# Kernel tuning notes

Hardware: AMD Instinct MI355X
Metric: run time of the kernel (lower is better)

Reference implementation:

```python
import jax, jax.numpy as jnp
import numpy as np

B, C, H, W = 16, 256, 96, 96
CQ = C // 8      # 32, query/key channels in CrossAttention
CM = C // 2      # 128, inter_planes


def conv1x1(x, w, b=None):
    # x: [B,Cin,H,W], w: [Cout,Cin]
    y = jnp.einsum('bchw,oc->bohw', x, w)
    if b is not None:
        y = y + b[None, :, None, None]
    return y


def cross_attention(x, wq, bq, wk, bk, wv, bv, gamma):
    # criss-cross (axial H and W) attention with -inf diagonal on the H branch
    b_, c_, h_, w_ = x.shape
    q = conv1x1(x, wq, bq)  # [B,CQ,H,W]
    k = conv1x1(x, wk, bk)
    v = conv1x1(x, wv, bv)  # [B,C,H,W]
    # energy over column (H axis): [B,H,W,H], masked diag h==h'
    e_h = jnp.einsum('bchw,bckw->bhwk', q, k)
    diag = jnp.eye(h_, dtype=bool)[None, :, None, :]  # [1,H,1,H]
    e_h = jnp.where(diag, -jnp.inf, e_h)
    # energy over row (W axis): [B,H,W,W]
    e_w = jnp.einsum('bchw,bchv->bhwv', q, k)
    att = jax.nn.softmax(jnp.concatenate([e_h, e_w], axis=3), axis=3)
    a_h, a_w = att[..., :h_], att[..., h_:]
    out_h = jnp.einsum('bckw,bhwk->bchw', v, a_h)
    out_w = jnp.einsum('bchv,bhwv->bchw', v, a_w)
    return gamma * (out_h + out_w) + x


def spatial_weighted(x, w_q_right, w_v_right, w_up, b_up):
    b_, _, h_, w_ = x.shape
    inp = conv1x1(x, w_v_right).reshape(b_, CM, h_ * w_)        # [B,CM,HW]
    mask = conv1x1(x, w_q_right).reshape(b_, 1, h_ * w_)        # [B,1,HW]
    mask = jax.nn.softmax(mask, axis=2)
    ctx = jnp.einsum('bcn,bon->bco', inp, mask)                 # [B,CM,1]
    ctx = jnp.einsum('bci,oc->boi', ctx, w_up) + b_up[None, :, None]  # [B,C,1]
    mask_ch = jax.nn.sigmoid(ctx)[..., None]                    # [B,C,1,1]
    return x * mask_ch


def channel_weighted(x, w_q_left, w_v_left):
    b_, _, h_, w_ = x.shape
    g = conv1x1(x, w_q_left)                                    # [B,CM,H,W]
    avg = jnp.mean(g, axis=(2, 3))                              # [B,CM]
    theta = conv1x1(x, w_v_left).reshape(b_, CM, h_ * w_)       # [B,CM,HW]
    ctx = jnp.einsum('bc,bcn->bn', avg, theta)                  # [B,HW]
    ctx = jax.nn.softmax(ctx, axis=1).reshape(b_, 1, h_, w_)
    return x * jax.nn.sigmoid(ctx)


def setup_inputs() -> dict:
    key = jax.random.key(0)
    ks = jax.random.split(key, 16)
    s = lambda fan_in: (2.0 / fan_in) ** 0.5
    inp = {
        'x': jax.random.normal(ks[0], (B, C, H, W), jnp.float32),
        'w_q_right': jax.random.normal(ks[1], (1, C), jnp.float32) * s(C),
        'w_v_right': jax.random.normal(ks[2], (CM, C), jnp.float32) * s(C),
        'w_up': jax.random.normal(ks[3], (C, CM), jnp.float32) * s(CM),
        'b_up': jnp.zeros((C,), jnp.float32),
        'w_q_left': jax.random.normal(ks[4], (CM, C), jnp.float32) * s(C),
        'w_v_left': jax.random.normal(ks[5], (CM, C), jnp.float32) * s(C),
        'cr_wq': jax.random.normal(ks[6], (CQ, C), jnp.float32) * s(C),
        'cr_bq': jnp.zeros((CQ,), jnp.float32),
        'cr_wk': jax.random.normal(ks[7], (CQ, C), jnp.float32) * s(C),
        'cr_bk': jnp.zeros((CQ,), jnp.float32),
        'cr_wv': jax.random.normal(ks[8], (C, C), jnp.float32) * s(C),
        'cr_bv': jnp.zeros((C,), jnp.float32),
        'gamma': jax.random.normal(ks[9], (1,), jnp.float32) * 0.1,
    }
    return inp


def reference(x, w_q_right, w_v_right, w_up, b_up, w_q_left, w_v_left,
              cr_wq, cr_bq, cr_wk, cr_bk, cr_wv, cr_bv, gamma):
    cross = lambda t: cross_attention(t, cr_wq, cr_bq, cr_wk, cr_bk, cr_wv, cr_bv, gamma)
    ctx_channel = cross(spatial_weighted(x, w_q_right, w_v_right, w_up, b_up))
    ctx_spatial = cross(channel_weighted(x, w_q_left, w_v_left))
    return cross(ctx_spatial + ctx_channel)
```

## Files before the change

kernel.cpp:

```cpp
#include <hip/hip_runtime.h>
#include <math.h>

#define Bn 16
#define Cn 256
#define CQn 32
#define CMn 128
#define Hn 96
#define Wn 96
#define Nn 9216
#define PIXn 147456

typedef short bf8 __attribute__((ext_vector_type(8)));
typedef float f32x4 __attribute__((ext_vector_type(4)));
#define MFMA(a,b,c) __builtin_amdgcn_mfma_f32_16x16x32_bf16(a,b,c,0,0,0)

typedef unsigned short ushort_t;

__device__ inline ushort_t f2bf(float f){
  union{float f; unsigned int u;} v; v.f=f;
  unsigned int r = v.u + 0x7fffu + ((v.u>>16)&1u);
  return (ushort_t)(r>>16);
}
__device__ inline float bf2f(ushort_t s){
  union{unsigned int u; float f;} v; v.u = ((unsigned int)s)<<16;
  return v.f;
}

__device__ inline float waveSum(float v){
#pragma unroll
  for(int o=32;o;o>>=1) v += __shfl_down(v,o,64);
  return v;
}
__device__ inline float waveMax(float v){
#pragma unroll
  for(int o=32;o;o>>=1) v = fmaxf(v,__shfl_down(v,o,64));
  return v;
}


__global__ __launch_bounds__(1024) void k_pass1(const float* __restrict__ x,
    const float* __restrict__ wqr, float* __restrict__ xmean,
    float* __restrict__ partp){
  int cg = blockIdx.x, b = blockIdx.y, tid = threadIdx.x;
  __shared__ float r16[16];
  float mp[9];
#pragma unroll
  for(int k=0;k<9;k++) mp[k]=0.f;
  for(int cc=0;cc<16;cc++){
    int c = cg*16+cc;
    const float* row = x + ((size_t)b*Cn + c)*Nn;
    float w = wqr[c];
    float s = 0.f;
#pragma unroll
    for(int k=0;k<9;k++){
      float v = row[k*1024+tid];
      s += v;
      mp[k] += w*v;
    }
    s = waveSum(s);
    if((tid&63)==0) r16[tid>>6]=s;
    __syncthreads();
    if(tid==0){
      float t=0.f;
      for(int i=0;i<16;i++) t+=r16[i];
      xmean[(size_t)b*Cn + c] = t*(1.f/Nn);
    }
    __syncthreads();
  }
  float* dst = partp + ((size_t)cg*Bn + b)*Nn;
#pragma unroll
  for(int k=0;k<9;k++) dst[k*1024+tid]=mp[k];
}

__global__ __launch_bounds__(1024) void k_pass2(const float* __restrict__ x,
    const float* __restrict__ wvec, const float* __restrict__ maskb,
    float* __restrict__ xw, float* __restrict__ partp){
  int cg = blockIdx.x, b = blockIdx.y, tid = threadIdx.x;
  __shared__ float r16[16];
  float cp[9], mk[9];
#pragma unroll
  for(int k=0;k<9;k++){
    cp[k]=0.f;
    mk[k]=maskb[(size_t)b*Nn + k*1024+tid];
  }
  for(int cc=0;cc<16;cc++){
    int c = cg*16+cc;
    const float* row = x + ((size_t)b*Cn + c)*Nn;
    float w = wvec[(size_t)b*Cn + c];
    float s = 0.f;
#pragma unroll
    for(int k=0;k<9;k++){
      float v = row[k*1024+tid];
      s += mk[k]*v;
      cp[k] += w*v;
    }
    s = waveSum(s);
    if((tid&63)==0) r16[tid>>6]=s;
    __syncthreads();
    if(tid==0){
      float t=0.f;
      for(int i=0;i<16;i++) t+=r16[i];
      xw[(size_t)b*Cn + c] = t;
    }
    __syncthreads();
  }
  float* dst = partp + ((size_t)cg*Bn + b)*Nn;
#pragma unroll
  for(int k=0;k<9;k++) dst[k*1024+tid]=cp[k];
}

__global__ void k_red16(const float* __restrict__ part, float* __restrict__ out){
  size_t p = (size_t)blockIdx.x*256 + threadIdx.x;
  float s=0.f;
#pragma unroll
  for(int cg=0;cg<16;cg++) s += part[(size_t)cg*Bn*Nn + p];
  out[p]=s;
}

__global__ void k_small1(const float* __restrict__ xmean, const float* __restrict__ wql,
                         const float* __restrict__ wvl, float* __restrict__ wvec){
  int b=blockIdx.x, t=threadIdx.x;
  __shared__ float xm[Cn];
  __shared__ float av[CMn];
  xm[t] = xmean[b*Cn+t];
  __syncthreads();
  if(t<CMn){
    float s=0.f;
    for(int c=0;c<Cn;c++) s += wql[t*Cn+c]*xm[c];
    av[t]=s;
  }
  __syncthreads();
  float s=0.f;
  for(int m=0;m<CMn;m++) s += av[m]*wvl[m*Cn+t];
  wvec[b*Cn+t]=s;
}

__global__ void k_softmax_n(const float* __restrict__ in, float* __restrict__ out, int mode){
  int b=blockIdx.x, tid=threadIdx.x, lane=tid&63, wid=tid>>6;
  const float* p = in + (size_t)b*Nn;
  __shared__ float red[16];
  __shared__ float bc2[2];
  float mx=-3e38f;
  for(int i=tid;i<Nn;i+=1024) mx=fmaxf(mx,p[i]);
  mx = waveMax(mx);
  if(lane==0) red[wid]=mx;
  __syncthreads();
  if(tid==0){ float m=red[0]; for(int i=1;i<16;i++) m=fmaxf(m,red[i]); bc2[0]=m; }
  __syncthreads();
  mx=bc2[0];
  float s=0.f;
  for(int i=tid;i<Nn;i+=1024) s+=expf(p[i]-mx);
  s = waveSum(s);
  __syncthreads();
  if(lane==0) red[wid]=s;
  __syncthreads();
  if(tid==0){ float t=0.f; for(int i=0;i<16;i++) t+=red[i]; bc2[1]=t; }
  __syncthreads();
  float inv=1.f/bc2[1];
  for(int i=tid;i<Nn;i+=1024){
    float e=expf(p[i]-mx)*inv;
    out[(size_t)b*Nn+i] = mode ? 1.f/(1.f+expf(-e)) : e;
  }
}

__global__ void k_small2(const float* __restrict__ xw, const float* __restrict__ wvr,
                         const float* __restrict__ wup, const float* __restrict__ bup,
                         float* __restrict__ g1){
  int b=blockIdx.x, t=threadIdx.x;
  __shared__ float xs[Cn];
  __shared__ float cx[CMn];
  xs[t]=xw[b*Cn+t];
  __syncthreads();
  if(t<CMn){
    float s=0.f;
    for(int c=0;c<Cn;c++) s += wvr[t*Cn+c]*xs[c];
    cx[t]=s;
  }
  __syncthreads();
  float s=bup[t];
  for(int m=0;m<CMn;m++) s += wup[t*CMn+m]*cx[m];
  g1[b*Cn+t]=1.f/(1.f+expf(-s));
}

__global__ void k_gates(const float* __restrict__ x, const float* __restrict__ g1,
                        const float* __restrict__ m2, ushort_t* __restrict__ t1,
                        ushort_t* __restrict__ t2){
  size_t i4 = ((size_t)blockIdx.x*256 + threadIdx.x)*4;
  int n  = (int)(i4 % Nn);
  int bc = (int)(i4 / Nn);
  int b  = bc / Cn;
  float4 xv = *(const float4*)&x[i4];
  float g = g1[bc];
  float4 mv = *(const float4*)&m2[(size_t)b*Nn + n];
  uint2 a, c;
  a.x = (unsigned)f2bf(xv.x*g) | ((unsigned)f2bf(xv.y*g)<<16);
  a.y = (unsigned)f2bf(xv.z*g) | ((unsigned)f2bf(xv.w*g)<<16);
  c.x = (unsigned)f2bf(xv.x*mv.x) | ((unsigned)f2bf(xv.y*mv.y)<<16);
  c.y = (unsigned)f2bf(xv.z*mv.z) | ((unsigned)f2bf(xv.w*mv.w)<<16);
  *(uint2*)&t1[i4] = a;
  *(uint2*)&t2[i4] = c;
}

__global__ void k_add_bf(ushort_t* __restrict__ a, const ushort_t* __restrict__ b){
  size_t i = ((size_t)blockIdx.x*256 + threadIdx.x)*8;
  uint4 av = *(const uint4*)&a[i];
  uint4 bv = *(const uint4*)&b[i];
  unsigned* ap = (unsigned*)&av; unsigned* bp2 = (unsigned*)&bv;
  uint4 ov;
  unsigned* op = (unsigned*)&ov;
#pragma unroll
  for(int k=0;k<4;k++){
    float lo = bf2f((ushort_t)(ap[k]&0xffff)) + bf2f((ushort_t)(bp2[k]&0xffff));
    float hi = bf2f((ushort_t)(ap[k]>>16))    + bf2f((ushort_t)(bp2[k]>>16));
    op[k] = (unsigned)f2bf(lo) | ((unsigned)f2bf(hi)<<16);
  }
  *(uint4*)&a[i] = ov;
}


__global__ void k_packb(const float* __restrict__ wq, const float* __restrict__ bq,
                        const float* __restrict__ wk, const float* __restrict__ bk,
                        const float* __restrict__ wv, const float* __restrict__ bv,
                        ushort_t* __restrict__ Wp, float* __restrict__ bp){
  int o = blockIdx.x, t = threadIdx.x;
  const float* src; float bs;
  if(o<32){ src = wq + o*Cn; bs = bq[o]; }
  else if(o<64){ src = wk + (o-32)*Cn; bs = bk[o-32]; }
  else { src = wv + (o-64)*Cn; bs = bv[o-64]; }
  Wp[o*Cn+t] = f2bf(src[t]);
  if(t==0) bp[o] = bs;
}

#define AP 40
#define BP 264

__global__ __launch_bounds__(256) void k_gemm_qkv(const ushort_t* __restrict__ x,
    const ushort_t* __restrict__ Wp, const float* __restrict__ bp,
    ushort_t* __restrict__ Yqk, ushort_t* __restrict__ Vb){
  __shared__ ushort_t Ws[320*AP];
  __shared__ ushort_t Bt[64*BP];
  int b  = blockIdx.y;
  int n0 = blockIdx.x*64;
  int tid = threadIdx.x, lane = tid&63, wid = tid>>6;

  {
    const ushort_t* xb = x + (size_t)b*Cn*Nn + n0 + (tid&63);
    int cg = (tid>>6)*8;
#pragma unroll
    for(int p=0;p<8;p++){
      int c8 = p*32 + cg;
      unsigned e0=xb[(size_t)(c8+0)*Nn], e1=xb[(size_t)(c8+1)*Nn];
      unsigned e2=xb[(size_t)(c8+2)*Nn], e3=xb[(size_t)(c8+3)*Nn];
      unsigned e4=xb[(size_t)(c8+4)*Nn], e5=xb[(size_t)(c8+5)*Nn];
      unsigned e6=xb[(size_t)(c8+6)*Nn], e7=xb[(size_t)(c8+7)*Nn];
      uint4 pk;
      pk.x = e0 | (e1<<16); pk.y = e2 | (e3<<16);
      pk.z = e4 | (e5<<16); pk.w = e6 | (e7<<16);
      *(uint4*)&Bt[(tid&63)*BP + c8] = pk;
    }
  }

  f32x4 acc[5][4];
#pragma unroll
  for(int f=0;f<5;f++)
#pragma unroll
    for(int g=0;g<4;g++) acc[f][g] = (f32x4){0.f,0.f,0.f,0.f};

  for(int ki=0;ki<8;ki++){
    __syncthreads();
#pragma unroll
    for(int q=0;q<5;q++){
      int fidx = q*256 + tid;
      int o = fidx>>2, kk = (fidx&3)*8;
      uint4 wv = *(const uint4*)&Wp[o*Cn + ki*32 + kk];
      *(uint4*)&Ws[o*AP + kk] = wv;
    }
    __syncthreads();
    bf8 bfr[4];
#pragma unroll
    for(int g=0;g<4;g++)
      bfr[g] = *(const bf8*)&Bt[(g*16 + (lane&15))*BP + ki*32 + (lane>>4)*8];
#pragma unroll
    for(int f=0;f<5;f++){
      bf8 a = *(const bf8*)&Ws[(wid*80 + f*16 + (lane&15))*AP + (lane>>4)*8];
#pragma unroll
      for(int g=0;g<4;g++) acc[f][g] = MFMA(a, bfr[g], acc[f][g]);
    }
  }

#pragma unroll
  for(int f=0;f<5;f++){
    int ob = wid*80 + f*16 + (lane>>4)*4;
#pragma unroll
    for(int i=0;i<4;i++){
      int o = ob + i;
      float bias = bp[o];
      ushort_t* dst = (o<64) ? (Yqk + ((size_t)b*64 + o)*Nn)
                             : (Vb + ((size_t)b*Cn + (o-64))*Nn);
#pragma unroll
      for(int g=0;g<4;g++)
        dst[n0 + g*16 + (lane&15)] = f2bf(acc[f][g][i] + bias);
    }
  }
}

__global__ __launch_bounds__(256) void k_transpose_b(const ushort_t* __restrict__ src,
                                                     ushort_t* __restrict__ dst){
  __shared__ ushort_t Ls[96*98];
  size_t base = (size_t)blockIdx.x * Nn;
  int tid = threadIdx.x;
  for(int e=tid*2; e<Nn; e+=512){
    unsigned int u = *(const unsigned int*)&src[base+e];
    int r=e/96, c=e%96;
    *(unsigned int*)&Ls[r*98+c] = u;
  }
  __syncthreads();
  for(int e=tid*2; e<Nn; e+=512){
    int r=e/96, c=e%96;
    unsigned int u = (unsigned int)Ls[c*98+r] | (((unsigned int)Ls[(c+1)*98+r])<<16);
    *(unsigned int*)&dst[base+e] = u;
  }
}

__global__ __launch_bounds__(256) void k_e(const ushort_t* __restrict__ Y,
    float* __restrict__ att, int aoff, int diag, int pm, int pr){
  __shared__ ushort_t Qt[96*AP];
  __shared__ ushort_t Kt[96*AP];
  int bid = blockIdx.x; int b = bid/96, r = bid%96;
  int tid = threadIdx.x, lane = tid&63, wid = tid>>6;
  {
    int half = tid>>7;
    int cg   = (tid>>5)&3;
    int l32  = tid&31;
    ushort_t* T = half ? Kt : Qt;
    const ushort_t* S = Y + ((size_t)b*64 + half*32 + cg*8)*Nn + (size_t)r*96;
#pragma unroll
    for(int p=0;p<3;p++){
      int sp = p*32 + l32;
      unsigned e0=S[(size_t)0*Nn+sp], e1=S[(size_t)1*Nn+sp];
      unsigned e2=S[(size_t)2*Nn+sp], e3=S[(size_t)3*Nn+sp];
      unsigned e4=S[(size_t)4*Nn+sp], e5=S[(size_t)5*Nn+sp];
      unsigned e6=S[(size_t)6*Nn+sp], e7=S[(size_t)7*Nn+sp];
      uint4 pk;
      pk.x = e0 | (e1<<16); pk.y = e2 | (e3<<16);
      pk.z = e4 | (e5<<16); pk.w = e6 | (e7<<16);
      *(uint4*)&T[sp*AP + cg*8] = pk;
    }
  }
  __syncthreads();
  int mb = (wid>>1)*48, nb = (wid&1)*48;
  const f32x4 z4 = {0.f,0.f,0.f,0.f};
  f32x4 acc[3][3];
  bf8 a[3], bb[3];
#pragma unroll
  for(int f=0;f<3;f++) a[f] = *(const bf8*)&Qt[(mb+f*16+(lane&15))*AP + (lane>>4)*8];
#pragma unroll
  for(int g=0;g<3;g++) bb[g] = *(const bf8*)&Kt[(nb+g*16+(lane&15))*AP + (lane>>4)*8];
#pragma unroll
  for(int f=0;f<3;f++)
#pragma unroll
    for(int g=0;g<3;g++) acc[f][g] = MFMA(a[f], bb[g], z4);
#pragma unroll
  for(int f=0;f<3;f++)
#pragma unroll
    for(int i=0;i<4;i++){
      int m = mb + f*16 + (lane>>4)*4 + i;
      float* arow = att + ((size_t)b*Nn + (size_t)m*pm + (size_t)r*pr)*192 + aoff;
#pragma unroll
      for(int g=0;g<3;g++){
        int n = nb + g*16 + (lane&15);
        arow[n] = (diag && n==m) ? -1e30f : acc[f][g][i];
      }
    }
}

__global__ void k_softmax_att(const float* __restrict__ att, ushort_t* __restrict__ attb){
  int wave = threadIdx.x>>6, lane = threadIdx.x&63;
  size_t p = (size_t)blockIdx.x*4 + wave;
  const float* a = att + p*192;
  float v0=a[lane], v1=a[lane+64], v2=a[lane+128];
  float mx = fmaxf(v0, fmaxf(v1,v2));
#pragma unroll
  for(int o=32;o;o>>=1) mx = fmaxf(mx, __shfl_xor(mx,o,64));
  float e0=expf(v0-mx), e1=expf(v1-mx), e2=expf(v2-mx);
  float s=e0+e1+e2;
#pragma unroll
  for(int o=32;o;o>>=1) s += __shfl_xor(s,o,64);
  float inv=1.f/s;
  ushort_t* ob = attb + p*192;
  ob[lane]     = f2bf(e0*inv);
  ob[lane+64]  = f2bf(e1*inv);
  ob[lane+128] = f2bf(e2*inv);
}

#define SP 120

template<int MODE, int OUTF>
__global__ __launch_bounds__(256) void k_pv(const ushort_t* V,
    const ushort_t* __restrict__ attb, const ushort_t* resid,
    float* __restrict__ Of, ushort_t* Ob, const float* __restrict__ gp){
  __shared__ ushort_t As[96*SP];
  int r = blockIdx.x, ch2 = blockIdx.y, b = blockIdx.z;
  float gm = gp[0];
  int tid = threadIdx.x, lane = tid&63, wid = tid>>6;
  size_t vbase = (size_t)b*Cn*Nn + (size_t)r*96;
  bf8 vf[6];
#pragma unroll
  for(int f=0;f<2;f++)
#pragma unroll
    for(int j=0;j<3;j++)
      vf[f*3+j] = *(const bf8*)&V[vbase
        + (size_t)(ch2*128 + wid*32 + f*16 + (lane&15))*Nn + j*32 + (lane>>4)*8];
  const ushort_t* ab = attb + (size_t)b*Nn*192
                     + (MODE ? (size_t)r*192 : (size_t)r*96*192 + 96);
  const size_t arow = MODE ? (size_t)96*192 : (size_t)192;
  for(int u=tid; u<96*12; u+=256){
    int n=u/12, j8=(u%12)*8;
    uint4 q = *(const uint4*)&ab[(size_t)n*arow + j8];
    *(uint4*)&As[n*SP + j8] = q;
  }
  __syncthreads();
  f32x4 acc[2][6];
#pragma unroll
  for(int f=0;f<2;f++)
#pragma unroll
    for(int g=0;g<6;g++) acc[f][g] = (f32x4){0.f,0.f,0.f,0.f};
#pragma unroll
  for(int j0=0;j0<3;j0++){
    bf8 bfr[6];
#pragma unroll
    for(int g=0;g<6;g++)
      bfr[g] = *(const bf8*)&As[(g*16+(lane&15))*SP + j0*32 + (lane>>4)*8];
#pragma unroll
    for(int f=0;f<2;f++)
#pragma unroll
      for(int g=0;g<6;g++) acc[f][g] = MFMA(vf[f*3+j0], bfr[g], acc[f][g]);
  }
#pragma unroll
  for(int f=0;f<2;f++){
    int cb = ch2*128 + wid*32 + f*16 + (lane>>4)*4;
#pragma unroll
    for(int i=0;i<4;i++){
      size_t row = vbase + (size_t)(cb+i)*Nn;
#pragma unroll
      for(int g=0;g<6;g++){
        int n = g*16 + (lane&15);
        float val = gm*acc[f][g][i];
        if(MODE==0) val += bf2f(resid[row+n]);
        if(OUTF) Of[row+n] = val;
        else     Ob[row+n] = f2bf(val);
      }
    }
  }
}

template<int OUTF>
__global__ __launch_bounds__(256) void k_merge(float* __restrict__ outf,
    ushort_t* __restrict__ outb, const ushort_t* __restrict__ OT){
  __shared__ ushort_t Ls[96*98];
  size_t base = (size_t)blockIdx.x * Nn;
  int tid = threadIdx.x;
  for(int e=tid*2; e<Nn; e+=512){
    unsigned int u = *(const unsigned int*)&OT[base+e];
    int r=e/96, c=e%96;
    *(unsigned int*)&Ls[r*98+c] = u;
  }
  __syncthreads();
  for(int e=tid*4; e<Nn; e+=1024){
    int r=e/96, c=e%96;
    if(OUTF){
      float4 o = *(float4*)&outf[base+e];
      o.x += bf2f(Ls[(c+0)*98+r]); o.y += bf2f(Ls[(c+1)*98+r]);
      o.z += bf2f(Ls[(c+2)*98+r]); o.w += bf2f(Ls[(c+3)*98+r]);
      *(float4*)&outf[base+e] = o;
    } else {
      uint2 u = *(uint2*)&outb[base+e];
      float a0 = bf2f((ushort_t)(u.x&0xffff)) + bf2f(Ls[(c+0)*98+r]);
      float a1 = bf2f((ushort_t)(u.x>>16))    + bf2f(Ls[(c+1)*98+r]);
      float a2 = bf2f((ushort_t)(u.y&0xffff)) + bf2f(Ls[(c+2)*98+r]);
      float a3 = bf2f((ushort_t)(u.y>>16))    + bf2f(Ls[(c+3)*98+r]);
      u.x = (unsigned)f2bf(a0) | ((unsigned)f2bf(a1)<<16);
      u.y = (unsigned)f2bf(a2) | ((unsigned)f2bf(a3)<<16);
      *(uint2*)&outb[base+e] = u;
    }
  }
}

extern "C" void kernel_launch(void* const* d_in, const int* in_sizes, int n_in,
                              void* d_out, int out_size, void* d_ws, size_t ws_size,
                              hipStream_t stream){
  const float* x    = (const float*)d_in[0];
  const float* wqr  = (const float*)d_in[1];
  const float* wvr  = (const float*)d_in[2];
  const float* wup  = (const float*)d_in[3];
  const float* bup  = (const float*)d_in[4];
  const float* wql  = (const float*)d_in[5];
  const float* wvl  = (const float*)d_in[6];
  const float* crwq = (const float*)d_in[7];
  const float* crbq = (const float*)d_in[8];
  const float* crwk = (const float*)d_in[9];
  const float* crbk = (const float*)d_in[10];
  const float* crwv = (const float*)d_in[11];
  const float* crbv = (const float*)d_in[12];
  const float* gma  = (const float*)d_in[13];
  float* out = (float*)d_out;

  const size_t XSZ = (size_t)Bn*Cn*Nn;
  const size_t YSZ = (size_t)Bn*64*Nn;
  char* wsb = (char*)d_ws;
  ushort_t* T1   = (ushort_t*)wsb; wsb += XSZ*2;
  ushort_t* T2   = (ushort_t*)wsb; wsb += XSZ*2;
  ushort_t* Vb   = (ushort_t*)wsb; wsb += XSZ*2;
  ushort_t* Yqk  = (ushort_t*)wsb; wsb += YSZ*2;
  ushort_t* Yqkt = (ushort_t*)wsb; wsb += YSZ*2;
  float*    ATT  = (float*)wsb;    wsb += (size_t)PIXn*192*4;
  ushort_t* ATTb = (ushort_t*)wsb; wsb += (size_t)PIXn*192*2;
  float*    partp= (float*)wsb;    wsb += (size_t)16*Bn*Nn*4;
  ushort_t* Wpb  = (ushort_t*)wsb; wsb += 320*Cn*2;
  float*    bp   = (float*)wsb;    wsb += 320*4;
  float*    xmean= (float*)wsb;    wsb += Bn*Cn*4;
  float*    wvec = (float*)wsb;    wsb += Bn*Cn*4;
  float*    xw   = (float*)wsb;    wsb += Bn*Cn*4;
  float*    g1   = (float*)wsb;    wsb += Bn*Cn*4;
  float*    mraw = (float*)wsb;    wsb += (size_t)PIXn*4;
  float*    maskb= (float*)wsb;    wsb += (size_t)PIXn*4;
  float*    craw = (float*)wsb;    wsb += (size_t)PIXn*4;
  float*    m2   = (float*)wsb;    wsb += (size_t)PIXn*4;

  k_packb<<<320,256,0,stream>>>(crwq,crbq,crwk,crbk,crwv,crbv,Wpb,bp);

  k_pass1<<<dim3(16,Bn),1024,0,stream>>>(x, wqr, xmean, partp);
  k_red16<<<Bn*Nn/256,256,0,stream>>>(partp, mraw);
  k_small1<<<Bn,256,0,stream>>>(xmean, wql, wvl, wvec);
  k_softmax_n<<<Bn,1024,0,stream>>>(mraw, maskb, 0);
  k_pass2<<<dim3(16,Bn),1024,0,stream>>>(x, wvec, maskb, xw, partp);
  k_red16<<<Bn*Nn/256,256,0,stream>>>(partp, craw);
  k_softmax_n<<<Bn,1024,0,stream>>>(craw, m2, 1);
  k_small2<<<Bn,256,0,stream>>>(xw, wvr, wup, bup, g1);
  k_gates<<<XSZ/1024,256,0,stream>>>(x, g1, m2, T1, T2);

  auto cross = [&](const ushort_t* t, ushort_t* ob, float* of, int finalf){
    k_gemm_qkv<<<dim3(Nn/64,Bn),256,0,stream>>>(t, Wpb, bp, Yqk, Vb);
    k_transpose_b<<<Bn*64,256,0,stream>>>(Yqk, Yqkt);
    k_e<<<Bn*96,256,0,stream>>>(Yqkt, ATT, 0, 1, 96, 1);
    k_e<<<Bn*96,256,0,stream>>>(Yqk,  ATT, 96, 0, 1, 96);
    k_softmax_att<<<PIXn/4,256,0,stream>>>(ATT, ATTb);
    if(finalf) k_pv<0,1><<<dim3(96,2,Bn),256,0,stream>>>(Vb, ATTb, t, of, nullptr, gma);
    else       k_pv<0,0><<<dim3(96,2,Bn),256,0,stream>>>(Vb, ATTb, t, nullptr, ob, gma);
    k_transpose_b<<<Bn*Cn,256,0,stream>>>(Vb, Vb);
    k_pv<1,0><<<dim3(96,2,Bn),256,0,stream>>>(Vb, ATTb, nullptr, nullptr, Vb, gma);
    if(finalf) k_merge<1><<<Bn*Cn,256,0,stream>>>(of, nullptr, Vb);
    else       k_merge<0><<<Bn*Cn,256,0,stream>>>(nullptr, ob, Vb);
  };

  cross(T1, T1, nullptr, 0);
  cross(T2, T2, nullptr, 0);
  k_add_bf<<<XSZ/2048,256,0,stream>>>(T1, T2);
  cross(T1, nullptr, out, 1);
}
```

Baseline: 1.301 ms.

## Merge axial attention launches, split attention layout, fuse residual add into merge

Computes the H and W energy tiles in one launch and writes softmax results into two separate bf16 buffers, with the H-branch stored already transposed per column. Both PV branches now run as a single 512-thread launch over all channels. V is transposed out of place into the freed fp32 energy buffer. The separate bf16 add of the two intermediate cross-attention outputs is folded into the second merge kernel. The aim is fewer launches, contiguous attention-row loads in PV, and one fewer full-tensor pass, at the cost of more workspace aliasing and scattered softmax stores for the H part.

New measurement: 1.222 ms. 1.07x faster.

```diff
diff --git a/kernel.cpp b/kernel.cpp
--- a/kernel.cpp
+++ b/kernel.cpp
@@ -201,22 +201,6 @@
   *(uint2*)&t2[i4] = c;
 }
 
-__global__ void k_add_bf(ushort_t* __restrict__ a, const ushort_t* __restrict__ b){
-  size_t i = ((size_t)blockIdx.x*256 + threadIdx.x)*8;
-  uint4 av = *(const uint4*)&a[i];
-  uint4 bv = *(const uint4*)&b[i];
-  unsigned* ap = (unsigned*)&av; unsigned* bp2 = (unsigned*)&bv;
-  uint4 ov;
-  unsigned* op = (unsigned*)&ov;
-#pragma unroll
-  for(int k=0;k<4;k++){
-    float lo = bf2f((ushort_t)(ap[k]&0xffff)) + bf2f((ushort_t)(bp2[k]&0xffff));
-    float hi = bf2f((ushort_t)(ap[k]>>16))    + bf2f((ushort_t)(bp2[k]>>16));
-    op[k] = (unsigned)f2bf(lo) | ((unsigned)f2bf(hi)<<16);
-  }
-  *(uint4*)&a[i] = ov;
-}
-
 
 __global__ void k_packb(const float* __restrict__ wq, const float* __restrict__ bq,
                         const float* __restrict__ wk, const float* __restrict__ bk,
@@ -322,11 +306,15 @@
   }
 }
 
-__global__ __launch_bounds__(256) void k_e(const ushort_t* __restrict__ Y,
-    float* __restrict__ att, int aoff, int diag, int pm, int pr){
+__global__ __launch_bounds__(256) void k_e2(const ushort_t* __restrict__ Yqk,
+    const ushort_t* __restrict__ Yqkt, float* __restrict__ att){
   __shared__ ushort_t Qt[96*AP];
   __shared__ ushort_t Kt[96*AP];
-  int bid = blockIdx.x; int b = bid/96, r = bid%96;
+  int r = blockIdx.x, mode = blockIdx.y, b = blockIdx.z;
+  const ushort_t* Y = mode ? Yqk : Yqkt;
+  int aoff = mode ? 96 : 0;
+  int pm   = mode ? 1  : 96;
+  int pr   = mode ? 96 : 1;
   int tid = threadIdx.x, lane = tid&63, wid = tid>>6;
   {
     int half = tid>>7;
@@ -360,6 +348,7 @@
   for(int f=0;f<3;f++)
 #pragma unroll
     for(int g=0;g<3;g++) acc[f][g] = MFMA(a[f], bb[g], z4);
+  int diag = (mode==0);
 #pragma unroll
   for(int f=0;f<3;f++)
 #pragma unroll
@@ -374,10 +363,11 @@
     }
 }
 
-__global__ void k_softmax_att(const float* __restrict__ att, ushort_t* __restrict__ attb){
+__global__ void k_softmax_att(const float* __restrict__ att,
+    ushort_t* __restrict__ attw, ushort_t* __restrict__ atth){
   int wave = threadIdx.x>>6, lane = threadIdx.x&63;
-  size_t p = (size_t)blockIdx.x*4 + wave;
-  const float* a = att + p*192;
+  int p = blockIdx.x*4 + wave;
+  const float* a = att + (size_t)p*192;
   float v0=a[lane], v1=a[lane+64], v2=a[lane+128];
   float mx = fmaxf(v0, fmaxf(v1,v2));
 #pragma unroll
@@ -387,22 +377,28 @@
 #pragma unroll
   for(int o=32;o;o>>=1) s += __shfl_xor(s,o,64);
   float inv=1.f/s;
-  ushort_t* ob = attb + p*192;
-  ob[lane]     = f2bf(e0*inv);
-  ob[lane+64]  = f2bf(e1*inv);
-  ob[lane+128] = f2bf(e2*inv);
+  int b = p/Nn, rem = p%Nn, h = rem/96, w = rem%96;
+  ushort_t* ph = atth + ((size_t)b*Nn + (size_t)w*96 + h)*96;
+  ushort_t* pw = attw + (size_t)p*96;
+  ph[lane] = f2bf(e0*inv);
+  if(lane<32) ph[64+lane] = f2bf(e1*inv);
+  else        pw[lane-32] = f2bf(e1*inv);
+  pw[lane+32] = f2bf(e2*inv);
 }
 
 #define SP 120
 
-template<int MODE, int OUTF>
-__global__ __launch_bounds__(256) void k_pv(const ushort_t* V,
-    const ushort_t* __restrict__ attb, const ushort_t* resid,
-    float* __restrict__ Of, ushort_t* Ob, const float* __restrict__ gp){
+template<int OUTF>
+__global__ __launch_bounds__(512) void k_pv2(const ushort_t* __restrict__ Vb,
+    const ushort_t* __restrict__ VT, const ushort_t* __restrict__ attw,
+    const ushort_t* __restrict__ atth, const ushort_t* resid,
+    float* __restrict__ Of, ushort_t* OwB, ushort_t* OT,
+    const float* __restrict__ gp){
   __shared__ ushort_t As[96*SP];
-  int r = blockIdx.x, ch2 = blockIdx.y, b = blockIdx.z;
+  int r = blockIdx.x, mode = blockIdx.y, b = blockIdx.z;
   float gm = gp[0];
   int tid = threadIdx.x, lane = tid&63, wid = tid>>6;
+  const ushort_t* V = mode ? VT : Vb;
   size_t vbase = (size_t)b*Cn*Nn + (size_t)r*96;
   bf8 vf[6];
 #pragma unroll
@@ -410,13 +406,11 @@
 #pragma unroll
     for(int j=0;j<3;j++)
       vf[f*3+j] = *(const bf8*)&V[vbase
-        + (size_t)(ch2*128 + wid*32 + f*16 + (lane&15))*Nn + j*32 + (lane>>4)*8];
-  const ushort_t* ab = attb + (size_t)b*Nn*192
-                     + (MODE ? (size_t)r*192 : (size_t)r*96*192 + 96);
-  const size_t arow = MODE ? (size_t)96*192 : (size_t)192;
-  for(int u=tid; u<96*12; u+=256){
+        + (size_t)(wid*32 + f*16 + (lane&15))*Nn + j*32 + (lane>>4)*8];
+  const ushort_t* ab = (mode ? atth : attw) + ((size_t)b*Nn + (size_t)r*96)*96;
+  for(int u=tid; u<96*12; u+=512){
     int n=u/12, j8=(u%12)*8;
-    uint4 q = *(const uint4*)&ab[(size_t)n*arow + j8];
+    uint4 q = *(const uint4*)&ab[n*96 + j8];
     *(uint4*)&As[n*SP + j8] = q;
   }
   __syncthreads();
@@ -438,25 +432,33 @@
   }
 #pragma unroll
   for(int f=0;f<2;f++){
-    int cb = ch2*128 + wid*32 + f*16 + (lane>>4)*4;
+    int cb = wid*32 + f*16 + (lane>>4)*4;
 #pragma unroll
     for(int i=0;i<4;i++){
       size_t row = vbase + (size_t)(cb+i)*Nn;
-#pragma unroll
-      for(int g=0;g<6;g++){
-        int n = g*16 + (lane&15);
-        float val = gm*acc[f][g][i];
-        if(MODE==0) val += bf2f(resid[row+n]);
-        if(OUTF) Of[row+n] = val;
-        else     Ob[row+n] = f2bf(val);
+      if(mode){
+#pragma unroll
+        for(int g=0;g<6;g++){
+          int n = g*16 + (lane&15);
+          OT[row+n] = f2bf(gm*acc[f][g][i]);
+        }
+      } else {
+#pragma unroll
+        for(int g=0;g<6;g++){
+          int n = g*16 + (lane&15);
+          float val = gm*acc[f][g][i] + bf2f(resid[row+n]);
+          if(OUTF) Of[row+n] = val;
+          else     OwB[row+n] = f2bf(val);
+        }
       }
     }
   }
 }
 
-template<int OUTF>
+template<int VAR>
 __global__ __launch_bounds__(256) void k_merge(float* __restrict__ outf,
-    ushort_t* __restrict__ outb, const ushort_t* __restrict__ OT){
+    ushort_t* __restrict__ outb, const ushort_t* __restrict__ add,
+    const ushort_t* __restrict__ OT){
   __shared__ ushort_t Ls[96*98];
   size_t base = (size_t)blockIdx.x * Nn;
   int tid = threadIdx.x;
@@ -468,17 +470,25 @@
   __syncthreads();
   for(int e=tid*4; e<Nn; e+=1024){
     int r=e/96, c=e%96;
-    if(OUTF){
+    float t0 = bf2f(Ls[(c+0)*98+r]), t1 = bf2f(Ls[(c+1)*98+r]);
+    float t2 = bf2f(Ls[(c+2)*98+r]), t3 = bf2f(Ls[(c+3)*98+r]);
+    if(VAR==1){
       float4 o = *(float4*)&outf[base+e];
-      o.x += bf2f(Ls[(c+0)*98+r]); o.y += bf2f(Ls[(c+1)*98+r]);
-      o.z += bf2f(Ls[(c+2)*98+r]); o.w += bf2f(Ls[(c+3)*98+r]);
+      o.x += t0; o.y += t1; o.z += t2; o.w += t3;
       *(float4*)&outf[base+e] = o;
     } else {
       uint2 u = *(uint2*)&outb[base+e];
-      float a0 = bf2f((ushort_t)(u.x&0xffff)) + bf2f(Ls[(c+0)*98+r]);
-      float a1 = bf2f((ushort_t)(u.x>>16))    + bf2f(Ls[(c+1)*98+r]);
-      float a2 = bf2f((ushort_t)(u.y&0xffff)) + bf2f(Ls[(c+2)*98+r]);
-      float a3 = bf2f((ushort_t)(u.y>>16))    + bf2f(Ls[(c+3)*98+r]);
+      float a0 = bf2f((ushort_t)(u.x&0xffff)) + t0;
+      float a1 = bf2f((ushort_t)(u.x>>16))    + t1;
+      float a2 = bf2f((ushort_t)(u.y&0xffff)) + t2;
+      float a3 = bf2f((ushort_t)(u.y>>16))    + t3;
+      if(VAR==2){
+        uint2 v = *(const uint2*)&add[base+e];
+        a0 += bf2f((ushort_t)(v.x&0xffff));
+        a1 += bf2f((ushort_t)(v.x>>16));
+        a2 += bf2f((ushort_t)(v.y&0xffff));
+        a3 += bf2f((ushort_t)(v.y>>16));
+      }
       u.x = (unsigned)f2bf(a0) | ((unsigned)f2bf(a1)<<16);
       u.y = (unsigned)f2bf(a2) | ((unsigned)f2bf(a3)<<16);
       *(uint2*)&outb[base+e] = u;
@@ -514,7 +524,9 @@
   ushort_t* Yqk  = (ushort_t*)wsb; wsb += YSZ*2;
   ushort_t* Yqkt = (ushort_t*)wsb; wsb += YSZ*2;
   float*    ATT  = (float*)wsb;    wsb += (size_t)PIXn*192*4;
-  ushort_t* ATTb = (ushort_t*)wsb; wsb += (size_t)PIXn*192*2;
+  ushort_t* VT   = (ushort_t*)ATT;
+  ushort_t* ATTw = (ushort_t*)wsb; wsb += (size_t)PIXn*96*2;
+  ushort_t* ATTh = (ushort_t*)wsb; wsb += (size_t)PIXn*96*2;
   float*    partp= (float*)wsb;    wsb += (size_t)16*Bn*Nn*4;
   ushort_t* Wpb  = (ushort_t*)wsb; wsb += 320*Cn*2;
   float*    bp   = (float*)wsb;    wsb += 320*4;
@@ -539,22 +551,20 @@
   k_small2<<<Bn,256,0,stream>>>(xw, wvr, wup, bup, g1);
   k_gates<<<XSZ/1024,256,0,stream>>>(x, g1, m2, T1, T2);
 
-  auto cross = [&](const ushort_t* t, ushort_t* ob, float* of, int finalf){
+  auto cross = [&](const ushort_t* t, ushort_t* ob, float* of, int var){
     k_gemm_qkv<<<dim3(Nn/64,Bn),256,0,stream>>>(t, Wpb, bp, Yqk, Vb);
     k_transpose_b<<<Bn*64,256,0,stream>>>(Yqk, Yqkt);
-    k_e<<<Bn*96,256,0,stream>>>(Yqkt, ATT, 0, 1, 96, 1);
-    k_e<<<Bn*96,256,0,stream>>>(Yqk,  ATT, 96, 0, 1, 96);
-    k_softmax_att<<<PIXn/4,256,0,stream>>>(ATT, ATTb);
-    if(finalf) k_pv<0,1><<<dim3(96,2,Bn),256,0,stream>>>(Vb, ATTb, t, of, nullptr, gma);
-    else       k_pv<0,0><<<dim3(96,2,Bn),256,0,stream>>>(Vb, ATTb, t, nullptr, ob, gma);
-    k_transpose_b<<<Bn*Cn,256,0,stream>>>(Vb, Vb);
-    k_pv<1,0><<<dim3(96,2,Bn),256,0,stream>>>(Vb, ATTb, nullptr, nullptr, Vb, gma);
-    if(finalf) k_merge<1><<<Bn*Cn,256,0,stream>>>(of, nullptr, Vb);
-    else       k_merge<0><<<Bn*Cn,256,0,stream>>>(nullptr, ob, Vb);
+    k_e2<<<dim3(96,2,Bn),256,0,stream>>>(Yqk, Yqkt, ATT);
+    k_softmax_att<<<PIXn/4,256,0,stream>>>(ATT, ATTw, ATTh);
+    k_transpose_b<<<Bn*Cn,256,0,stream>>>(Vb, VT);
+    if(var==1) k_pv2<1><<<dim3(96,2,Bn),512,0,stream>>>(Vb, VT, ATTw, ATTh, t, of, nullptr, VT, gma);
+    else       k_pv2<0><<<dim3(96,2,Bn),512,0,stream>>>(Vb, VT, ATTw, ATTh, t, nullptr, ob, VT, gma);
+    if(var==0)      k_merge<0><<<Bn*Cn,256,0,stream>>>(nullptr, ob, nullptr, VT);
+    else if(var==1) k_merge<1><<<Bn*Cn,256,0,stream>>>(of, nullptr, nullptr, VT);
+    else            k_merge<2><<<Bn*Cn,256,0,stream>>>(nullptr, T1, T2, VT);
   };
 
   cross(T1, T1, nullptr, 0);
-  cross(T2, T2, nullptr, 0);
-  k_add_bf<<<XSZ/2048,256,0,stream>>>(T1, T2);
+  cross(T2, T2, nullptr, 2);
   cross(T1, nullptr, out, 1);
 }
```
